# Optimization experiments

Hardware: AMD Instinct MI355X
Metric: run time of the kernel (lower is better)

## Reference

```python
import jax, jax.numpy as jnp
import numpy as np

B, T, V = 128, 128, 30000
DE, DP, PV = 300, 30, 50
H = 300
HEADS = 6
LA, LL = 5, 24
POL = 3
RED = 10
NEG = -1e9


def entmax15(x):
    # exact 1.5-entmax along last axis (sorting algorithm, Peters & Martins 2019)
    d = x.shape[-1]
    x = x / 2.0
    x = x - jnp.max(x, axis=-1, keepdims=True)
    xs = -jnp.sort(-x, axis=-1)                      # descending
    rho = jnp.arange(1, d + 1, dtype=x.dtype)
    mean = jnp.cumsum(xs, axis=-1) / rho
    meansq = jnp.cumsum(xs * xs, axis=-1) / rho
    ss = rho * (meansq - mean * mean)
    delta = (1.0 - ss) / rho
    tau = mean - jnp.sqrt(jnp.maximum(delta, 0.0))
    support = jnp.sum((tau <= xs).astype(jnp.int32), axis=-1, keepdims=True)
    tau_star = jnp.take_along_axis(tau, support - 1, axis=-1)
    return jnp.square(jnp.maximum(x - tau_star, 0.0))


def lstm_dir(x, mask, Wih, Whh, bih, bhh, reverse):
    # packed-sequence-equivalent LSTM: state frozen / output zeroed at padded steps
    b = x.shape[0]
    h0 = jnp.zeros((b, Whh.shape[1]), x.dtype)

    def step(carry, inp):
        h, c = carry
        xt, mt = inp
        g = xt @ Wih.T + h @ Whh.T + (bih + bhh)
        i, f, gg, o = jnp.split(g, 4, axis=-1)       # torch gate order i,f,g,o
        c_new = jax.nn.sigmoid(f) * c + jax.nn.sigmoid(i) * jnp.tanh(gg)
        h_new = jax.nn.sigmoid(o) * jnp.tanh(c_new)
        m = mt[:, None]
        return (jnp.where(m, h_new, h), jnp.where(m, c_new, c)), jnp.where(m, h_new, 0.0)

    _, outs = jax.lax.scan(step, (h0, h0),
                           (jnp.swapaxes(x, 0, 1), jnp.swapaxes(mask, 0, 1)),
                           reverse=reverse)
    return jnp.swapaxes(outs, 0, 1)


def se_layer(x, valid, w1, b1, w2, b2):
    # SELayer over the SEQUENCE dim (channel == max_len); x: [b,t,d], valid: [b,t]
    y = jnp.mean(x, axis=-1)                         # adaptive avg-pool over (1, d)
    y = jax.nn.relu(y @ w1.T + b1) @ w2.T + b2
    y = y + jnp.where(valid > 0, 0.0, NEG)           # mask_2
    y = jax.nn.softmax(y, axis=1)
    return x * y[..., None]


def gcn(x, A, W, b):
    # D @ A @ D @ x @ W + b with D = diag((rowsum(A)+1)^-0.5)
    dn = (jnp.sum(A, axis=2) + 1.0) ** -0.5
    An = dn[:, :, None] * A * dn[:, None, :]
    return jnp.einsum('bij,bjd->bid', An, x) @ W + b


def _forward(text_indices, aspect_indices, left_indices, pos_indices, asp_post, height,
             adj, embed_matrix, pos_emb_w, Wih_f, Whh_f, bih_f, bhh_f,
             Wih_b, Whh_b, bih_b, bhh_b, wq, bq, wk, bk,
             se_w1, se_b1, se_w2, se_b2, gc1_w, gc1_b, gc2_w, gc2_b,
             affine1, affine2, fc_w, fc_b):
    b, t = text_indices.shape
    nonpad = text_indices != 0
    valid = nonpad.astype(jnp.float32)               # mask_ squeezed -> [b,t]
    text_len = jnp.sum(nonpad, axis=-1)
    aspect_real_len = jnp.sum(aspect_indices != 0, axis=-1)
    left_len = jnp.sum(left_indices != 0, axis=-1)   # aspect_double_idx = [left_len,left_len]

    # embedding; overwrite aspect position with mean aspect embedding
    text = embed_matrix[text_indices]
    am = (aspect_indices != 0).astype(jnp.float32)[..., None]
    asp_mean = jnp.sum(embed_matrix[aspect_indices] * am, axis=1) / aspect_real_len[:, None].astype(jnp.float32)
    text = text.at[jnp.arange(b), asp_post].set(asp_mean)
    embs = jnp.concatenate([text, pos_emb_w[pos_indices]], axis=-1)

    lenmask = jnp.arange(t)[None, :] < text_len[:, None]
    text_out = jnp.concatenate([
        lstm_dir(embs, lenmask, Wih_f, Whh_f, bih_f, bhh_f, False),
        lstm_dir(embs, lenmask, Wih_b, Whh_b, bih_b, bhh_b, True)], axis=-1)  # [b,t,2H]

    # multi-head entmax attention -> semantic adjacency
    dk = (2 * H) // HEADS
    q = (text_out @ wq.T + bq).reshape(b, t, HEADS, dk).transpose(0, 2, 1, 3)
    k = (text_out @ wk.T + bk).reshape(b, t, HEADS, dk).transpose(0, 2, 1, 3)
    scores = jnp.einsum('bhqd,bhkd->bhqk', q, k) / (dk ** 0.5)
    scores = jnp.where(nonpad[:, None, None, :], scores, NEG)
    adj_sem = jnp.mean(entmax15(scores), axis=1)     # average over heads
    eye = jnp.eye(t, dtype=adj_sem.dtype)
    adj_sem = adj_sem * (1.0 - eye) + eye            # zero diagonal, add identity
    adj_sem = valid[:, :, None] * adj_sem

    se = lambda z: se_layer(z, valid, se_w1, se_b1, se_w2, se_b2)
    # (the first x = relu(gc1(..,adj)); x = relu(gc2(..,adj)) branch is dead code:
    #  x is overwritten before use, so only the x_sem path matters)
    x_sem = jax.nn.relu(gcn(se(text_out), adj_sem, gc1_w, gc1_b))
    x = jax.nn.relu(gcn(se(x_sem), adj, gc2_w, gc2_b))

    A1 = jax.nn.softmax(jnp.einsum('bid,bjd->bij', x @ affine1, x_sem), axis=-1)
    A2 = jax.nn.softmax(jnp.einsum('bid,bjd->bij', x_sem @ affine2, x), axis=-1)
    out = jnp.concatenate([jnp.einsum('bij,bjd->bid', A1, x_sem),
                           jnp.einsum('bij,bjd->bid', A2, x)], axis=-1)  # [b,t,4H]
    aspmask = (jnp.arange(t)[None, :] == left_len[:, None]).astype(jnp.float32)
    pooled = jnp.sum(out * aspmask[..., None], axis=1)  # keep aspect token only
    return pooled @ fc_w + fc_b                         # [b, POL]


def setup_inputs():
    key = jax.random.key(0)
    ks = jax.random.split(key, 36)
    f32 = jnp.float32
    pos_t = jnp.arange(T)[None, :]
    text_len = jax.random.randint(ks[0], (B,), T // 2, T + 1)
    text_indices = jax.random.randint(ks[1], (B, T), 1, V) * (pos_t < text_len[:, None])
    asp_len = jax.random.randint(ks[2], (B,), 1, LA + 1)
    aspect_indices = jax.random.randint(ks[3], (B, LA), 1, V) * (jnp.arange(LA)[None, :] < asp_len[:, None])
    left_len = jax.random.randint(ks[4], (B,), 1, LL + 1)
    left_indices = jax.random.randint(ks[5], (B, LL), 1, V) * (jnp.arange(LL)[None, :] < left_len[:, None])
    pos_indices = jax.random.randint(ks[6], (B, T), 1, PV) * (pos_t < text_len[:, None])
    vmask = (pos_t < text_len[:, None]).astype(f32)
    adj = (jax.random.uniform(ks[7], (B, T, T)) < 0.08).astype(f32)
    adj = adj * vmask[:, :, None] * vmask[:, None, :]
    asp_post = left_len                              # aspect sits right after left context
    height = jax.random.randint(ks[8], (B, T + 1), 1, 12)

    def rn(k, shape, scale=0.05):
        return jax.random.normal(k, shape, dtype=f32) * scale

    params = dict(
        embed_matrix=rn(ks[9], (V, DE), 0.5),
        pos_emb_w=rn(ks[10], (PV, DP), 0.5).at[0].set(0.0),
        Wih_f=rn(ks[11], (4 * H, DE + DP)), Whh_f=rn(ks[12], (4 * H, H)),
        bih_f=rn(ks[13], (4 * H,)), bhh_f=rn(ks[14], (4 * H,)),
        Wih_b=rn(ks[15], (4 * H, DE + DP)), Whh_b=rn(ks[16], (4 * H, H)),
        bih_b=rn(ks[17], (4 * H,)), bhh_b=rn(ks[18], (4 * H,)),
        wq=rn(ks[19], (2 * H, 2 * H)), bq=rn(ks[20], (2 * H,)),
        wk=rn(ks[21], (2 * H, 2 * H)), bk=rn(ks[22], (2 * H,)),
        se_w1=rn(ks[23], (T // RED, T)), se_b1=rn(ks[24], (T // RED,)),
        se_w2=rn(ks[25], (T, T // RED)), se_b2=rn(ks[26], (T,)),
        gc1_w=rn(ks[27], (2 * H, 2 * H)), gc1_b=rn(ks[28], (2 * H,)),
        gc2_w=rn(ks[29], (2 * H, 2 * H)), gc2_b=rn(ks[30], (2 * H,)),
        affine1=rn(ks[31], (2 * H, 2 * H)), affine2=rn(ks[32], (2 * H, 2 * H)),
        fc_w=rn(ks[33], (4 * H, POL)), fc_b=rn(ks[34], (POL,)),
    )
    return dict(text_indices=text_indices, aspect_indices=aspect_indices,
                left_indices=left_indices, pos_indices=pos_indices,
                asp_post=asp_post, height=height, adj=adj, **params)


def reference(text_indices, aspect_indices, left_indices, pos_indices, asp_post, height,
              adj, embed_matrix, pos_emb_w, Wih_f, Whh_f, bih_f, bhh_f,
              Wih_b, Whh_b, bih_b, bhh_b, wq, bq, wk, bk,
              se_w1, se_b1, se_w2, se_b2, gc1_w, gc1_b, gc2_w, gc2_b,
              affine1, affine2, fc_w, fc_b):
    return _forward(text_indices, aspect_indices, left_indices, pos_indices, asp_post, height,
                    adj, embed_matrix, pos_emb_w, Wih_f, Whh_f, bih_f, bhh_f,
                    Wih_b, Whh_b, bih_b, bhh_b, wq, bq, wk, bk,
                    se_w1, se_b1, se_w2, se_b2, gc1_w, gc1_b, gc2_w, gc2_b,
                    affine1, affine2, fc_w, fc_b)
```

## Files before the change

### kernel.cpp

```cpp
#include <hip/hip_runtime.h>

typedef unsigned short ushort_t;
typedef unsigned int   uint_t;
typedef __attribute__((ext_vector_type(8))) short short8;
typedef __attribute__((ext_vector_type(4))) float floatx4;

#define NEGV -1000000000.0f

__device__ __forceinline__ float bf2f(ushort_t h){ return __uint_as_float(((uint_t)h)<<16); }
__device__ __forceinline__ ushort_t f2bf(float f){
  uint_t u = __float_as_uint(f);
  uint_t r = u + 0x7fffu + ((u>>16)&1u);
  return (ushort_t)(r>>16);
}
__device__ __forceinline__ float wredsum(float v){ for(int o=32;o;o>>=1) v += __shfl_xor(v,o); return v; }
__device__ __forceinline__ float wredmax(float v){ for(int o=32;o;o>>=1) v = fmaxf(v,__shfl_xor(v,o)); return v; }
__device__ __forceinline__ int   wredsumi(int v){ for(int o=32;o;o>>=1) v += __shfl_xor(v,o); return v; }

__device__ __forceinline__ short8 ldg_cohr(const ushort_t* p){
  short8 r;
  asm volatile("global_load_dwordx4 %0, %1, off sc0 sc1"
               : "=&v"(r) : "v"(p) : "memory");
  return r;
}
__device__ __forceinline__ void stg_b128_cohr(ushort_t* p, short8 v){
  asm volatile("global_store_dwordx4 %0, %1, off sc0 sc1" :: "v"(p), "v"(v) : "memory");
}

__device__ __forceinline__ float fsig(float x){ return 1.f/(1.f+__expf(-x)); }
__device__ __forceinline__ float ftanh(float x){ return 1.f - 2.f/(1.f+__expf(2.f*x)); }

__global__ void k_cvt8(const void* __restrict__ src, ushort_t* __restrict__ dst,
                       long n, const ushort_t* __restrict__ probe_src){
  __shared__ int sflag;
  if (threadIdx.x < 64){
    ushort_t u = probe_src[2*threadIdx.x];
    int e = (u>>7)&0xFF;
    int c = (e>=100 && e<=140) ? 1 : 0;
    c = wredsumi(c);
    if (threadIdx.x==0) sflag = (c>32) ? 1 : 0;
  }
  __syncthreads();
  bool isbf = (sflag!=0);
  long base = (blockIdx.x*256L + threadIdx.x)*8;
  if (base>=n) return;
  if (isbf){
    if (base+8<=n) *(uint4*)(dst+base) = *(const uint4*)((const ushort_t*)src+base);
    else for (long i=base;i<n;i++) dst[i]=((const ushort_t*)src)[i];
  } else {
    const float* s = (const float*)src;
    if (base+8<=n){
      float4 v0 = *(const float4*)(s+base);
      float4 v1 = *(const float4*)(s+base+4);
      ushort_t o[8] = {f2bf(v0.x),f2bf(v0.y),f2bf(v0.z),f2bf(v0.w),
                       f2bf(v1.x),f2bf(v1.y),f2bf(v1.z),f2bf(v1.w)};
      *(uint4*)(dst+base) = *(uint4*)o;
    } else {
      for (long i=base;i<n;i++) dst[i]=f2bf(s[i]);
    }
  }
}

__device__ __forceinline__ bool probe_is_bf16(const ushort_t* probe_src){
  int c=0;
  #pragma unroll 1
  for (int i=0;i<64;i++){
    ushort_t u = probe_src[2*i];
    int e = (u>>7)&0xFF;
    c += (e>=100 && e<=140) ? 1 : 0;
  }
  return c>32;
}

__global__ void k_lens(const int* __restrict__ ti, const int* __restrict__ li,
                       int* __restrict__ nonpad, int* __restrict__ text_len,
                       int* __restrict__ left_len){
  int b = blockIdx.x, t = threadIdx.x;
  nonpad[b*128+t] = (ti[b*128+t]!=0) ? 1 : 0;
  if (t==0){
    int c=0; for (int k2=0;k2<128;k2++) c += (ti[b*128+k2]!=0);
    text_len[b]=c;
    int l=0; for (int k2=0;k2<24;k2++) l += (li[b*24+k2]!=0);
    left_len[b]=l;
  }
}

__global__ void k_aspmean(const int* __restrict__ ai, const ushort_t* __restrict__ em,
                          float* __restrict__ asp_mean){
  int b = blockIdx.x;
  int idxs[5]; int cnt=0;
  for (int a=0;a<5;a++){ int ix=ai[b*5+a]; idxs[a]=ix; cnt += (ix!=0); }
  float inv = 1.0f/(float)cnt;
  for (int d=threadIdx.x; d<300; d+=128){
    float s=0.f;
    for (int a=0;a<5;a++) if (idxs[a]) s += bf2f(em[(long)idxs[a]*300+d]);
    asp_mean[b*300+d] = s*inv;
  }
}

__global__ void k_embs(const int* __restrict__ ti, const int* __restrict__ pi,
                       const int* __restrict__ asp_post,
                       const ushort_t* __restrict__ em, const ushort_t* __restrict__ pe,
                       const float* __restrict__ asp_mean, ushort_t* __restrict__ embs){
  int blk = blockIdx.x;
  int b = blk>>7, t = blk&127;
  int ap = asp_post[b];
  int tix = ti[b*128+t];
  int pix = pi[b*128+t];
  for (int col=threadIdx.x; col<336; col+=128){
    ushort_t v;
    if (col<300) v = (t==ap) ? f2bf(asp_mean[b*300+col]) : em[(long)tix*300+col];
    else if (col<330) v = pe[pix*30 + (col-300)];
    else v = 0;
    embs[(long)(b*128+t)*336 + col] = v;
  }
}

__global__ void k_padwih2(const ushort_t* __restrict__ src, ushort_t* __restrict__ dst){
  int i = blockIdx.x*blockDim.x + threadIdx.x;
  if (i >= 1280*336) return;
  int r = i/336, k = i - r*336;
  int j = r>>2, gate = r&3;
  ushort_t v = 0;
  if (j<300 && k<330) v = src[(long)(gate*300+j)*330 + k];
  dst[i] = v;
}

__global__ void k_padwhh2(const ushort_t* __restrict__ src, ushort_t* __restrict__ dst){
  int i = blockIdx.x*blockDim.x + threadIdx.x;
  if (i >= 1280*320) return;
  int r = i/320, k = i - r*320;
  int j = r>>2, gate = r&3;
  ushort_t v = 0;
  if (j<300 && k<300) v = src[(long)(gate*300+j)*300 + k];
  dst[i] = v;
}

__global__ void k_biassum2(const ushort_t* __restrict__ a, const ushort_t* __restrict__ b,
                           float* __restrict__ dst){
  int i = blockIdx.x*blockDim.x + threadIdx.x;
  if (i>=1280) return;
  int j = i>>2, g = i&3;
  dst[i] = (j<300) ? (bf2f(a[g*300+j]) + bf2f(b[g*300+j])) : 0.f;
}

__global__ void k_biascvt(const ushort_t* __restrict__ a, float* __restrict__ dst, int n){
  int i = blockIdx.x*blockDim.x + threadIdx.x;
  if (i<n) dst[i] = bf2f(a[i]);
}

template<int TB, int MODE>
__global__ __launch_bounds__(256) void gemm_k(
    int M, int N, int K,
    const ushort_t* __restrict__ A, long lda, long sAz,
    const ushort_t* __restrict__ B, long ldb, long sBz,
    float* __restrict__ Cf, ushort_t* __restrict__ Cb, long ldc, long sCz,
    const float* __restrict__ bias, int relu,
    const float* __restrict__ rowscale,
    const int* __restrict__ nonpad)
{
  __shared__ ushort_t As[128*40];
  __shared__ ushort_t Bs[128*40];
  const int tid = threadIdx.x;
  const int m0 = blockIdx.x*128, n0 = blockIdx.y*128;
  const int z = blockIdx.z;
  const ushort_t* Ap = A + (long)z*sAz;
  const ushort_t* Bp = B + (long)z*sBz;
  floatx4 acc[4][4];
  #pragma unroll
  for (int i=0;i<4;i++)
    #pragma unroll
    for (int j=0;j<4;j++){ acc[i][j][0]=0.f; acc[i][j][1]=0.f; acc[i][j][2]=0.f; acc[i][j][3]=0.f; }
  const int w = tid>>6, wm = w&1, wn = w>>1;
  const int lane = tid&63, lr = lane&15, lq = lane>>4;

  for (int k0=0;k0<K;k0+=32){
    #pragma unroll
    for (int c2=0;c2<2;c2++){
      int ch = tid + 256*c2;
      int row = ch>>2, kc = (ch&3)*8;
      int gr = m0+row, gk = k0+kc;
      uint4 v{};
      if (gr<M && gk<K) v = *(const uint4*)(Ap + (long)gr*lda + gk);
      *(uint4*)(&As[row*40+kc]) = v;
    }
    if (TB){
      #pragma unroll
      for (int c2=0;c2<2;c2++){
        int ch = tid + 256*c2;
        int row = ch>>2, kc = (ch&3)*8;
        int gn = n0+row, gk = k0+kc;
        uint4 v{};
        if (gn<N && gk<K) v = *(const uint4*)(Bp + (long)gn*ldb + gk);
        int sw = kc ^ (((row>>3)&3)<<3);
        *(uint4*)(&Bs[row*40+sw]) = v;
      }
    } else {
      #pragma unroll
      for (int c2=0;c2<2;c2++){
        int ch = tid + 256*c2;
        int kk = ch>>4, nc = (ch&15)*8;
        int gk = k0+kk, gn = n0+nc;
        uint4 v{};
        if (gk<K && gn<N) v = *(const uint4*)(Bp + (long)gk*ldb + gn);
        uint_t wsv[4] = {v.x, v.y, v.z, v.w};
        #pragma unroll
        for (int e=0;e<8;e++){
          ushort_t hv = (e&1) ? (ushort_t)(wsv[e>>1]>>16) : (ushort_t)(wsv[e>>1]&0xffffu);
          int n = nc+e;
          int sw = kk ^ (((n>>3)&3)<<3);
          Bs[n*40+sw] = hv;
        }
      }
    }
    __syncthreads();
    short8 af[4], bfv[4];
    #pragma unroll
    for (int i=0;i<4;i++) af[i] = *(const short8*)(&As[(wm*64+i*16+lr)*40 + lq*8]);
    #pragma unroll
    for (int j=0;j<4;j++){
      int n = wn*64+j*16+lr;
      int sw = (lq*8) ^ (((n>>3)&3)<<3);
      bfv[j] = *(const short8*)(&Bs[n*40+sw]);
    }
    #pragma unroll
    for (int i=0;i<4;i++)
      #pragma unroll
      for (int j=0;j<4;j++)
        acc[i][j] = __builtin_amdgcn_mfma_f32_16x16x32_bf16(af[i], bfv[j], acc[i][j], 0,0,0);
    __syncthreads();
  }

  #pragma unroll
  for (int i=0;i<4;i++){
    #pragma unroll
    for (int j=0;j<4;j++){
      #pragma unroll
      for (int r=0;r<4;r++){
        int row = m0 + wm*64 + i*16 + lq*4 + r;
        int col = n0 + wn*64 + j*16 + lr;
        if (row<M && col<N){
          float v = acc[i][j][r];
          if (rowscale) v *= rowscale[(long)z*M + row];
          if (bias) v += bias[col];
          if (relu && v<0.f) v = 0.f;
          if (MODE==1){
            Cb[(long)z*sCz + (long)row*ldc + col] = f2bf(v);
          } else if (MODE==2){
            int b = row>>7, t = row&127;
            int h = col/100, d = col - h*100;
            Cb[ ((long)((b*6+h)*128+t))*104 + d ] = f2bf(v);
          } else if (MODE==3){
            v *= 0.1f;
            if (!nonpad[(z/6)*128 + col]) v = NEGV;
            Cf[(long)z*sCz + (long)row*ldc + col] = v;
          }
        }
      }
    }
  }
}

#define ALD 328
#define HXD 40

__global__ __launch_bounds__(512,1) void lstm2_k(
    const ushort_t* __restrict__ whh2f, const ushort_t* __restrict__ whh2b,
    const ushort_t* __restrict__ gipf, const ushort_t* __restrict__ gipb,
    ushort_t* __restrict__ hbuf,
    int* __restrict__ barr,
    ushort_t* __restrict__ text_out, const int* __restrict__ text_len)
{
  __shared__ ushort_t Alds[128*ALD];
  __shared__ ushort_t Blds[64*ALD];
  __shared__ ushort_t hx[64*HXD];

  const int bx = blockIdx.x;
  const int slice = bx % 10;
  const int grp   = bx / 10;
  const int dir = grp & 1, bh = grp >> 1;
  const ushort_t* __restrict__ whh = dir ? whh2b : whh2f;
  const ushort_t* __restrict__ gip = dir ? gipb : gipf;
  ushort_t* hb = hbuf + (long)dir * (2L*128*320);
  int* bar = barr + grp*128;

  const int tid = threadIdx.x;
  const int w = tid>>6, lane = tid&63, lr = lane&15, lq = lane>>4;
  const int wm = w&3, wn = w>>2;

  for (int i = tid; i < 128*40; i += 512){
    int row = i/40, c = (i-row*40)*8;
    uint4 v = *(const uint4*)(whh + (long)(slice*128+row)*320 + c);
    *(uint4*)(&Alds[row*ALD + c]) = v;
  }

  int jj_[2], b_[2], bl_[2], tl_[2];
  #pragma unroll
  for (int mi=0;mi<2;mi++) jj_[mi] = slice*32 + wm*8 + mi*4 + lq;
  #pragma unroll
  for (int ni=0;ni<2;ni++){
    bl_[ni] = wn*32 + ni*16 + lr;
    b_[ni]  = bh*64 + bl_[ni];
    tl_[ni] = text_len[b_[ni]];
  }

  const int aoff0 = ((wm*2+0)*16+lr)*ALD + lq*8;
  const int aoff1 = ((wm*2+1)*16+lr)*ALD + lq*8;
  const int boff0 = (wn*32+   lr)*ALD + lq*8;
  const int boff1 = (wn*32+16+lr)*ALD + lq*8;

  float    c_st[2][2];
  ushort_t h_st[2][2];
  #pragma unroll
  for (int mi=0;mi<2;mi++){ c_st[mi][0]=0.f; c_st[mi][1]=0.f; h_st[mi][0]=0; h_st[mi][1]=0; }

  __syncthreads();

  for (int s=0; s<128; s++){
    const int t = dir ? (127-s) : s;
    const ushort_t* rb = hb + (long)(s&1)*(128L*320);
    ushort_t*       wb = hb + (long)((s+1)&1)*(128L*320);

    uint2 gp[2][2];
    #pragma unroll
    for (int mi=0;mi<2;mi++)
      #pragma unroll
      for (int ni=0;ni<2;ni++)
        gp[mi][ni] = *(const uint2*)(gip + ((long)(b_[ni]*128 + t))*1280 + jj_[mi]*4);

    short8 tmp[5]; int ro_[5], ch_[5];
    #pragma unroll
    for (int k=0;k<5;k++){
      int c = tid + k*512;
      int row = c/40, ch = c - row*40;
      ro_[k]=row; ch_[k]=ch;
      tmp[k] = ldg_cohr(rb + (long)(bh*64+row)*320 + ch*8);
    }
    asm volatile("s_waitcnt vmcnt(0)" ::: "memory");
    __builtin_amdgcn_sched_barrier(0);
    #pragma unroll
    for (int k=0;k<5;k++)
      *(short8*)(&Blds[ro_[k]*ALD + ch_[k]*8]) = tmp[k];
    __syncthreads();

    floatx4 acc[2][2];
    #pragma unroll
    for (int mi=0;mi<2;mi++)
      #pragma unroll
      for (int ni=0;ni<2;ni++){ acc[mi][ni][0]=0.f; acc[mi][ni][1]=0.f; acc[mi][ni][2]=0.f; acc[mi][ni][3]=0.f; }
    #pragma unroll
    for (int kf=0;kf<10;kf++){
      short8 a0 = *(const short8*)(&Alds[aoff0 + kf*32]);
      short8 a1 = *(const short8*)(&Alds[aoff1 + kf*32]);
      short8 b0 = *(const short8*)(&Blds[boff0 + kf*32]);
      short8 b1 = *(const short8*)(&Blds[boff1 + kf*32]);
      acc[0][0] = __builtin_amdgcn_mfma_f32_16x16x32_bf16(a0, b0, acc[0][0], 0,0,0);
      acc[0][1] = __builtin_amdgcn_mfma_f32_16x16x32_bf16(a0, b1, acc[0][1], 0,0,0);
      acc[1][0] = __builtin_amdgcn_mfma_f32_16x16x32_bf16(a1, b0, acc[1][0], 0,0,0);
      acc[1][1] = __builtin_amdgcn_mfma_f32_16x16x32_bf16(a1, b1, acc[1][1], 0,0,0);
    }

    #pragma unroll
    for (int mi=0;mi<2;mi++){
      #pragma unroll
      for (int ni=0;ni<2;ni++){
        float g_i = acc[mi][ni][0] + bf2f((ushort_t)(gp[mi][ni].x & 0xffffu));
        float g_f = acc[mi][ni][1] + bf2f((ushort_t)(gp[mi][ni].x >> 16));
        float g_g = acc[mi][ni][2] + bf2f((ushort_t)(gp[mi][ni].y & 0xffffu));
        float g_o = acc[mi][ni][3] + bf2f((ushort_t)(gp[mi][ni].y >> 16));
        float ig = fsig(g_i);
        float fg = fsig(g_f);
        float gg = ftanh(g_g);
        float og = fsig(g_o);
        float cn = fg*c_st[mi][ni] + ig*gg;
        float hn = og*ftanh(cn);
        bool m = (t < tl_[ni]);
        if (m) c_st[mi][ni] = cn;
        ushort_t hv = m ? f2bf(hn) : h_st[mi][ni];
        h_st[mi][ni] = hv;
        hx[bl_[ni]*HXD + wm*8 + mi*4 + lq] = hv;
        if (jj_[mi] < 300)
          text_out[((long)(b_[ni]*128 + t))*600 + dir*300 + jj_[mi]] = m ? f2bf(hn) : (ushort_t)0;
      }
    }
    __syncthreads();

    if (tid < 256){
      int row = tid>>2, jj8 = (tid&3)*8;
      short8 hvv = *(const short8*)(&hx[row*HXD + jj8]);
      stg_b128_cohr(wb + (long)(bh*64+row)*320 + slice*32 + jj8, hvv);
    }
    asm volatile("s_waitcnt vmcnt(0)" ::: "memory");
    __syncthreads();
    if (tid==0){
      __hip_atomic_fetch_add(&bar[s], 1, __ATOMIC_RELAXED, __HIP_MEMORY_SCOPE_AGENT);
      while (__hip_atomic_load(&bar[s], __ATOMIC_RELAXED, __HIP_MEMORY_SCOPE_AGENT) < 10)
        __builtin_amdgcn_s_sleep(1);
    }
    __syncthreads();
  }
}

__global__ __launch_bounds__(64) void k_entmax(float* __restrict__ p){
  long row = blockIdx.x;
  float* base = p + row*128;
  __shared__ float xo[128], xs[128], c1[128], c2[128];
  int t = threadIdx.x;
  float a = base[t]*0.5f, b = base[t+64]*0.5f;
  float m = wredmax(fmaxf(a,b));
  a -= m; b -= m;
  xo[t]=a; xo[t+64]=b; xs[t]=a; xs[t+64]=b;
  __syncthreads();
  for (int k2=2;k2<=128;k2<<=1){
    for (int j=k2>>1;j>0;j>>=1){
      int i = ((t & ~(j-1))<<1) | (t & (j-1));
      int ixj = i | j;
      float vi = xs[i], vj = xs[ixj];
      bool blk = (i & k2)==0;
      bool sw = blk ? (vi < vj) : (vi > vj);
      __syncthreads();
      if (sw){ xs[i]=vj; xs[ixj]=vi; }
      __syncthreads();
    }
  }
  c1[t]=xs[t];       c2[t]=xs[t]*xs[t];
  c1[t+64]=xs[t+64]; c2[t+64]=xs[t+64]*xs[t+64];
  __syncthreads();
  for (int d=1; d<128; d<<=1){
    float a1 = (t>=d)     ? c1[t-d]    : 0.f;
    float a2 = (t>=d)     ? c2[t-d]    : 0.f;
    float b1 = (t+64>=d)  ? c1[t+64-d] : 0.f;
    float b2 = (t+64>=d)  ? c2[t+64-d] : 0.f;
    float x1=c1[t], y1=c2[t], x2=c1[t+64], y2=c2[t+64];
    __syncthreads();
    c1[t]=x1+a1; c2[t]=y1+a2; c1[t+64]=x2+b1; c2[t+64]=y2+b2;
    __syncthreads();
  }
  float tau_a, tau_b; int cnt=0;
  {
    float rho = (float)(t+1);
    float mean = c1[t]/rho, msq = c2[t]/rho;
    float ss = rho*(msq-mean*mean);
    float delta = (1.f-ss)/rho;
    tau_a = mean - sqrtf(fmaxf(delta,0.f));
    cnt += (tau_a <= xs[t]) ? 1 : 0;
  }
  {
    float rho = (float)(t+65);
    float mean = c1[t+64]/rho, msq = c2[t+64]/rho;
    float ss = rho*(msq-mean*mean);
    float delta = (1.f-ss)/rho;
    tau_b = mean - sqrtf(fmaxf(delta,0.f));
    cnt += (tau_b <= xs[t+64]) ? 1 : 0;
  }
  __syncthreads();
  c1[t]=tau_a; c1[t+64]=tau_b;
  __syncthreads();
  int support = wredsumi(cnt);
  support = (support<1) ? 1 : ((support>128) ? 128 : support);
  float tau_star = c1[support-1];
  float oa = fmaxf(xo[t]-tau_star, 0.f);
  float ob = fmaxf(xo[t+64]-tau_star, 0.f);
  base[t] = oa*oa; base[t+64] = ob*ob;
}

__global__ void k_adjsem(const float* __restrict__ p, const int* __restrict__ nonpad,
                         ushort_t* __restrict__ adj_sem){
  int idx = blockIdx.x*blockDim.x + threadIdx.x;
  if (idx >= 128*128*128) return;
  int b = idx>>14, rem = idx&16383, i = rem>>7, j = rem&127;
  float s = 0.f;
  for (int h=0;h<6;h++) s += p[(long)b*98304 + h*16384 + i*128 + j];
  float v = s/6.0f;
  if (i==j) v = 1.0f;
  if (!nonpad[b*128+i]) v = 0.f;
  adj_sem[idx] = f2bf(v);
}

__global__ __launch_bounds__(64) void k_dn(const ushort_t* __restrict__ src, float* __restrict__ dnv){
  long row = blockIdx.x;
  int l = threadIdx.x;
  float s = bf2f(src[row*128+l]) + bf2f(src[row*128+l+64]);
  s = wredsum(s);
  if (l==0) dnv[row] = 1.0f/sqrtf(s+1.0f);
}

__global__ __launch_bounds__(64) void k_mean(const ushort_t* __restrict__ X, float* __restrict__ ymean){
  long row = blockIdx.x;
  float s=0.f;
  for (int d=threadIdx.x; d<600; d+=64) s += bf2f(X[row*600+d]);
  s = wredsum(s);
  if (threadIdx.x==0) ymean[row] = s/600.0f;
}

__global__ void k_senet(const float* __restrict__ ymean,
                        const ushort_t* __restrict__ w1, const ushort_t* __restrict__ b1,
                        const ushort_t* __restrict__ w2, const ushort_t* __restrict__ b2,
                        const int* __restrict__ nonpad, float* __restrict__ ysoft){
  int b = blockIdx.x, t = threadIdx.x;
  __shared__ float yv[128], z1[12], red[128];
  yv[t] = ymean[b*128+t];
  __syncthreads();
  if (t<12){
    float s = bf2f(b1[t]);
    for (int k2=0;k2<128;k2++) s += yv[k2]*bf2f(w1[t*128+k2]);
    z1[t] = fmaxf(s,0.f);
  }
  __syncthreads();
  float v = bf2f(b2[t]);
  for (int r=0;r<12;r++) v += z1[r]*bf2f(w2[t*12+r]);
  if (!nonpad[b*128+t]) v += NEGV;
  red[t]=v; __syncthreads();
  for (int s2=64;s2>0;s2>>=1){ if (t<s2) red[t]=fmaxf(red[t],red[t+s2]); __syncthreads(); }
  float mx = red[0]; __syncthreads();
  float e = expf(v-mx);
  red[t]=e; __syncthreads();
  for (int s2=64;s2>0;s2>>=1){ if (t<s2) red[t]+=red[t+s2]; __syncthreads(); }
  float sm = red[0];
  ysoft[b*128+t] = e/sm;
}

__global__ void k_scale2(const ushort_t* __restrict__ X, const float* __restrict__ ysoft,
                         const float* __restrict__ dnv, ushort_t* __restrict__ out){
  int i = blockIdx.x*blockDim.x + threadIdx.x;
  if (i >= 128*128*600) return;
  int row = i/600;
  out[i] = f2bf(bf2f(X[i])*ysoft[row]*dnv[row]);
}

__global__ void k_gather(const ushort_t* __restrict__ X, const int* __restrict__ left_len,
                         ushort_t* __restrict__ dst){
  int b = blockIdx.x;
  int lb = left_len[b];
  for (int d=threadIdx.x; d<600; d+=128)
    dst[b*600+d] = X[(long)(b*128+lb)*600+d];
}

__global__ __launch_bounds__(256) void k_pool(const ushort_t* __restrict__ g,
                                              const ushort_t* __restrict__ X,
                                              float* __restrict__ pooled, int poff){
  int b = blockIdx.x, tid = threadIdx.x;
  __shared__ float gs[600], sbuf[128], red[256];
  for (int d=tid; d<600; d+=256) gs[d] = bf2f(g[b*600+d]);
  __syncthreads();
  int wv = tid>>6, lane = tid&63;
  for (int jj=wv; jj<128; jj+=4){
    float s=0.f;
    for (int d=lane; d<600; d+=64) s += gs[d]*bf2f(X[(long)(b*128+jj)*600+d]);
    s = wredsum(s);
    if (lane==0) sbuf[jj]=s;
  }
  __syncthreads();
  float v = (tid<128) ? sbuf[tid] : -3.4e38f;
  red[tid]=v; __syncthreads();
  for (int s2=128;s2>0;s2>>=1){ if (tid<s2) red[tid]=fmaxf(red[tid],red[tid+s2]); __syncthreads(); }
  float mx = red[0]; __syncthreads();
  float e = (tid<128) ? expf(v-mx) : 0.f;
  red[tid]=e; __syncthreads();
  for (int s2=128;s2>0;s2>>=1){ if (tid<s2) red[tid]+=red[tid+s2]; __syncthreads(); }
  float sm = red[0]; __syncthreads();
  if (tid<128) sbuf[tid] = e/sm;
  __syncthreads();
  for (int d=tid; d<600; d+=256){
    float acc=0.f;
    for (int j=0;j<128;j++) acc += sbuf[j]*bf2f(X[(long)(b*128+j)*600+d]);
    pooled[(long)b*1200 + poff + d] = acc;
  }
}

__global__ __launch_bounds__(64) void k_final(const float* __restrict__ pooled,
                                              const ushort_t* __restrict__ fcw,
                                              const ushort_t* __restrict__ fcb,
                                              void* __restrict__ out,
                                              const ushort_t* __restrict__ probe_src){
  bool isbf = probe_is_bf16(probe_src);
  int b = blockIdx.x, lane = threadIdx.x;
  for (int p=0;p<3;p++){
    float s=0.f;
    for (int d=lane; d<1200; d+=64) s += pooled[(long)b*1200+d]*bf2f(fcw[d*3+p]);
    s = wredsum(s);
    if (lane==0){
      float r = s + bf2f(fcb[p]);
      if (isbf) ((ushort_t*)out)[b*3+p] = f2bf(r);
      else      ((float*)out)[b*3+p] = r;
    }
  }
}

extern "C" void kernel_launch(void* const* d_in, const int* in_sizes, int n_in,
                              void* d_out, int out_size, void* d_ws, size_t ws_size,
                              hipStream_t stream) {
  const int*      ti   = (const int*)d_in[0];
  const int*      ai   = (const int*)d_in[1];
  const int*      li   = (const int*)d_in[2];
  const int*      pi   = (const int*)d_in[3];
  const int*      aps  = (const int*)d_in[4];
  const ushort_t* probe = (const ushort_t*)d_in[7];

  char* w = (char*)d_ws; size_t off = 0;
  auto alloc = [&](size_t bytes)->char*{ char* p = w+off; off = (off+bytes+255)&~(size_t)255; return p; };

  int*   text_len = (int*)alloc(512);
  int*   left_len = (int*)alloc(512);
  int*   nonpad   = (int*)alloc(65536);
  float* asp_mean = (float*)alloc(153600);
  float* dn1      = (float*)alloc(65536);
  float* dn2      = (float*)alloc(65536);
  float* ymean    = (float*)alloc(65536);
  float* ysoft    = (float*)alloc(65536);
  ushort_t* wihpf = (ushort_t*)alloc(860160);
  ushort_t* wihpb = (ushort_t*)alloc(860160);
  ushort_t* whh2f = (ushort_t*)alloc(819200);
  ushort_t* whh2b = (ushort_t*)alloc(819200);
  ushort_t* hbuf  = (ushort_t*)alloc(327680);
  int*      barr  = (int*)alloc(2048);
  float* biasgf   = (float*)alloc(5120);
  float* biasgb   = (float*)alloc(5120);
  float* bqf      = (float*)alloc(2400);
  float* bkf      = (float*)alloc(2400);
  float* gc1bf    = (float*)alloc(2400);
  float* gc2bf    = (float*)alloc(2400);
  ushort_t* g1    = (ushort_t*)alloc(153600);
  ushort_t* g2    = (ushort_t*)alloc(153600);
  ushort_t* xr    = (ushort_t*)alloc(153600);
  ushort_t* xsr   = (ushort_t*)alloc(153600);
  float* pooled   = (float*)alloc(614400);
  ushort_t* adj_c  = (ushort_t*)alloc(4194304);
  ushort_t* pe_c   = (ushort_t*)alloc(2048);
  ushort_t* wihf_c = (ushort_t*)alloc(792000);
  ushort_t* wihb_c = (ushort_t*)alloc(792000);
  ushort_t* whhf_c = (ushort_t*)alloc(720000);
  ushort_t* whhb_c = (ushort_t*)alloc(720000);
  ushort_t* bihf_c = (ushort_t*)alloc(2400);
  ushort_t* bhhf_c = (ushort_t*)alloc(2400);
  ushort_t* bihb_c = (ushort_t*)alloc(2400);
  ushort_t* bhhb_c = (ushort_t*)alloc(2400);
  ushort_t* wq_c   = (ushort_t*)alloc(720000);
  ushort_t* bq_c   = (ushort_t*)alloc(1200);
  ushort_t* wk_c   = (ushort_t*)alloc(720000);
  ushort_t* bk_c   = (ushort_t*)alloc(1200);
  ushort_t* sw1_c  = (ushort_t*)alloc(3072);
  ushort_t* sb1_c  = (ushort_t*)alloc(256);
  ushort_t* sw2_c  = (ushort_t*)alloc(3072);
  ushort_t* sb2_c  = (ushort_t*)alloc(256);
  ushort_t* g1w_c  = (ushort_t*)alloc(720000);
  ushort_t* g1b_c  = (ushort_t*)alloc(1200);
  ushort_t* g2w_c  = (ushort_t*)alloc(720000);
  ushort_t* g2b_c  = (ushort_t*)alloc(1200);
  ushort_t* af1_c  = (ushort_t*)alloc(720000);
  ushort_t* af2_c  = (ushort_t*)alloc(720000);
  ushort_t* fcw_c  = (ushort_t*)alloc(7200);
  ushort_t* fcb_c  = (ushort_t*)alloc(256);
  ushort_t* embs  = (ushort_t*)alloc(11010048);
  ushort_t* textout = (ushort_t*)alloc(19660800);
  char* R = alloc(95420416);
  ushort_t* em_c    = (ushort_t*)(R);
  ushort_t* gip_f   = (ushort_t*)(R);
  ushort_t* gip_b   = (ushort_t*)(R+41943040);
  ushort_t* qh      = (ushort_t*)(R);
  ushort_t* kh      = (ushort_t*)(R+20447232);
  float*    scores  = (float*)(R+40894464);
  ushort_t* adj_sem = (ushort_t*)(R+91226112);
  ushort_t* se_x    = (ushort_t*)(R+40894464);
  ushort_t* Zb      = (ushort_t*)(R+60555264);
  ushort_t* x_sem   = (ushort_t*)(R);
  ushort_t* xb      = (ushort_t*)(R+20447232);
  (void)ws_size; (void)n_in; (void)in_sizes; (void)out_size;

  {
    const int idx[27] = {7,6, 8,9,13,10,14,11,12,15,16,17,18,19,20,21,22,23,24,25,26,27,28,29,30,31,32};
    ushort_t* dl[27] = {em_c,adj_c, pe_c,wihf_c,wihb_c,whhf_c,whhb_c,bihf_c,bhhf_c,bihb_c,bhhb_c,
                        wq_c,bq_c,wk_c,bk_c,sw1_c,sb1_c,sw2_c,sb2_c,
                        g1w_c,g1b_c,g2w_c,g2b_c,af1_c,af2_c,fcw_c,fcb_c};
    const long nl[27] = {9000000L,2097152L, 900,396000,396000,360000,360000,1200,1200,1200,1200,
                         360000,600,360000,600,1536,12,1536,128,
                         360000,600,360000,600,360000,360000,3600,3};
    for (int i=0;i<27;i++){
      long nb = ((nl[i]+7)/8 + 255)/256;
      k_cvt8<<<(int)nb,256,0,stream>>>(d_in[idx[i]], dl[i], nl[i], probe);
    }
  }

  k_lens<<<128,128,0,stream>>>(ti, li, nonpad, text_len, left_len);
  k_aspmean<<<128,128,0,stream>>>(ai, em_c, asp_mean);
  k_embs<<<16384,128,0,stream>>>(ti, pi, aps, em_c, pe_c, asp_mean, embs);
  k_padwih2<<<(1280*336+255)/256,256,0,stream>>>(wihf_c, wihpf);
  k_padwih2<<<(1280*336+255)/256,256,0,stream>>>(wihb_c, wihpb);
  k_padwhh2<<<(1280*320+255)/256,256,0,stream>>>(whhf_c, whh2f);
  k_padwhh2<<<(1280*320+255)/256,256,0,stream>>>(whhb_c, whh2b);
  k_biassum2<<<(1280+255)/256,256,0,stream>>>(bihf_c, bhhf_c, biasgf);
  k_biassum2<<<(1280+255)/256,256,0,stream>>>(bihb_c, bhhb_c, biasgb);
  k_biascvt<<<3,256,0,stream>>>(bq_c, bqf, 600);
  k_biascvt<<<3,256,0,stream>>>(bk_c, bkf, 600);
  k_biascvt<<<3,256,0,stream>>>(g1b_c, gc1bf, 600);
  k_biascvt<<<3,256,0,stream>>>(g2b_c, gc2bf, 600);

  gemm_k<1,1><<<dim3(128,10,1),256,0,stream>>>(16384,1280,336, embs,336,0, wihpf,336,0,
        nullptr, gip_f,1280,0, biasgf,0,nullptr,nullptr);
  gemm_k<1,1><<<dim3(128,10,1),256,0,stream>>>(16384,1280,336, embs,336,0, wihpb,336,0,
        nullptr, gip_b,1280,0, biasgb,0,nullptr,nullptr);

  hipMemsetAsync(hbuf, 0, 327680, stream);
  hipMemsetAsync(barr, 0, 2048, stream);
  lstm2_k<<<40,512,0,stream>>>(whh2f, whh2b, gip_f, gip_b, hbuf, barr, textout, text_len);

  hipMemsetAsync(qh, 0, 20447232, stream);
  hipMemsetAsync(kh, 0, 20447232, stream);
  gemm_k<1,2><<<dim3(128,5,1),256,0,stream>>>(16384,600,600, textout,600,0, wq_c,600,0,
        nullptr, qh,0,0, bqf,0,nullptr,nullptr);
  gemm_k<1,2><<<dim3(128,5,1),256,0,stream>>>(16384,600,600, textout,600,0, wk_c,600,0,
        nullptr, kh,0,0, bkf,0,nullptr,nullptr);

  gemm_k<1,3><<<dim3(1,1,768),256,0,stream>>>(128,128,104, qh,104,13312, kh,104,13312,
        scores, nullptr, 128, 16384, nullptr,0,nullptr, nonpad);

  k_entmax<<<98304,64,0,stream>>>(scores);

  k_adjsem<<<(2097152+255)/256,256,0,stream>>>(scores, nonpad, adj_sem);
  k_dn<<<16384,64,0,stream>>>(adj_sem, dn1);
  k_dn<<<16384,64,0,stream>>>(adj_c, dn2);

  k_mean<<<16384,64,0,stream>>>(textout, ymean);
  k_senet<<<128,128,0,stream>>>(ymean, sw1_c,sb1_c,sw2_c,sb2_c, nonpad, ysoft);
  k_scale2<<<(9830400+255)/256,256,0,stream>>>(textout, ysoft, dn1, se_x);
  gemm_k<0,1><<<dim3(1,5,128),256,0,stream>>>(128,600,128, adj_sem,128,16384, se_x,600,76800,
        nullptr, Zb,600,76800, nullptr,0, dn1, nullptr);
  gemm_k<0,1><<<dim3(128,5,1),256,0,stream>>>(16384,600,600, Zb,600,0, g1w_c,600,0,
        nullptr, x_sem,600,0, gc1bf,1,nullptr,nullptr);

  k_mean<<<16384,64,0,stream>>>(x_sem, ymean);
  k_senet<<<128,128,0,stream>>>(ymean, sw1_c,sb1_c,sw2_c,sb2_c, nonpad, ysoft);
  k_scale2<<<(9830400+255)/256,256,0,stream>>>(x_sem, ysoft, dn2, se_x);
  gemm_k<0,1><<<dim3(1,5,128),256,0,stream>>>(128,600,128, adj_c,128,16384, se_x,600,76800,
        nullptr, Zb,600,76800, nullptr,0, dn2, nullptr);
  gemm_k<0,1><<<dim3(128,5,1),256,0,stream>>>(16384,600,600, Zb,600,0, g2w_c,600,0,
        nullptr, xb,600,0, gc2bf,1,nullptr,nullptr);

  k_gather<<<128,128,0,stream>>>(xb, left_len, xr);
  k_gather<<<128,128,0,stream>>>(x_sem, left_len, xsr);
  gemm_k<0,1><<<dim3(1,5,1),256,0,stream>>>(128,600,600, xr,600,0, af1_c,600,0,
        nullptr, g1,600,0, nullptr,0,nullptr,nullptr);
  gemm_k<0,1><<<dim3(1,5,1),256,0,stream>>>(128,600,600, xsr,600,0, af2_c,600,0,
        nullptr, g2,600,0, nullptr,0,nullptr,nullptr);
  k_pool<<<128,256,0,stream>>>(g1, x_sem, pooled, 0);
  k_pool<<<128,256,0,stream>>>(g2, xb, pooled, 600);

  k_final<<<128,64,0,stream>>>(pooled, fcw_c, fcb_c, d_out, probe);
}
```

Measured before the change: 1.867 ms.

## Keep LSTM recurrent weights in registers and prefetch next-step gate inputs

The persistent LSTM kernel now loads each wave's slice of the recurrent weight matrix into registers once, instead of staging it in LDS and reading it back every step. The per-step precomputed gate inputs for the next timestep are prefetched at the end of the current step, so that load overlaps the barrier wait. The text_out stores are made unconditional through a dummy buffer, so the s_waitcnt can use a fixed count, vmcnt(8), and no longer drains them. The goal is to shorten the serial per-step critical path, at the cost of higher register pressure and reliance on an exact in-flight memory operation count.

```diff
diff --git a/kernel.cpp b/kernel.cpp
--- a/kernel.cpp
+++ b/kernel.cpp
@@ -261,7 +261,7 @@
   }
 }
 
-#define ALD 328
+#define BLD 328
 #define HXD 40
 
 __global__ __launch_bounds__(512,1) void lstm2_k(
@@ -269,10 +269,10 @@
     const ushort_t* __restrict__ gipf, const ushort_t* __restrict__ gipb,
     ushort_t* __restrict__ hbuf,
     int* __restrict__ barr,
-    ushort_t* __restrict__ text_out, const int* __restrict__ text_len)
+    ushort_t* __restrict__ text_out, const int* __restrict__ text_len,
+    ushort_t* __restrict__ dumpb)
 {
-  __shared__ ushort_t Alds[128*ALD];
-  __shared__ ushort_t Blds[64*ALD];
+  __shared__ ushort_t Blds[64*BLD];
   __shared__ ushort_t hx[64*HXD];
 
   const int bx = blockIdx.x;
@@ -288,11 +288,18 @@
   const int w = tid>>6, lane = tid&63, lr = lane&15, lq = lane>>4;
   const int wm = w&3, wn = w>>2;
 
-  for (int i = tid; i < 128*40; i += 512){
-    int row = i/40, c = (i-row*40)*8;
-    uint4 v = *(const uint4*)(whh + (long)(slice*128+row)*320 + c);
-    *(uint4*)(&Alds[row*ALD + c]) = v;
-  }
+  short8 a[2][10];
+  #pragma unroll
+  for (int mi=0;mi<2;mi++){
+    const ushort_t* ar = whh + (long)(slice*128 + (wm*2+mi)*16 + lr)*320 + lq*8;
+    #pragma unroll
+    for (int kf=0;kf<10;kf++) a[mi][kf] = *(const short8*)(ar + kf*32);
+  }
+  #pragma unroll
+  for (int mi=0;mi<2;mi++)
+    #pragma unroll
+    for (int kf=0;kf<10;kf++)
+      asm volatile("" : "+v"(a[mi][kf]));
 
   int jj_[2], b_[2], bl_[2], tl_[2];
   #pragma unroll
@@ -304,29 +311,28 @@
     tl_[ni] = text_len[b_[ni]];
   }
 
-  const int aoff0 = ((wm*2+0)*16+lr)*ALD + lq*8;
-  const int aoff1 = ((wm*2+1)*16+lr)*ALD + lq*8;
-  const int boff0 = (wn*32+   lr)*ALD + lq*8;
-  const int boff1 = (wn*32+16+lr)*ALD + lq*8;
+  const int boff0 = (wn*32+   lr)*BLD + lq*8;
+  const int boff1 = (wn*32+16+lr)*BLD + lq*8;
 
   float    c_st[2][2];
   ushort_t h_st[2][2];
   #pragma unroll
   for (int mi=0;mi<2;mi++){ c_st[mi][0]=0.f; c_st[mi][1]=0.f; h_st[mi][0]=0; h_st[mi][1]=0; }
 
-  __syncthreads();
+  uint2 gp[2][2];
+  {
+    int t0 = dir ? 127 : 0;
+    #pragma unroll
+    for (int mi=0;mi<2;mi++)
+      #pragma unroll
+      for (int ni=0;ni<2;ni++)
+        gp[mi][ni] = *(const uint2*)(gip + ((long)(b_[ni]*128 + t0))*1280 + jj_[mi]*4);
+  }
 
   for (int s=0; s<128; s++){
     const int t = dir ? (127-s) : s;
     const ushort_t* rb = hb + (long)(s&1)*(128L*320);
     ushort_t*       wb = hb + (long)((s+1)&1)*(128L*320);
-
-    uint2 gp[2][2];
-    #pragma unroll
-    for (int mi=0;mi<2;mi++)
-      #pragma unroll
-      for (int ni=0;ni<2;ni++)
-        gp[mi][ni] = *(const uint2*)(gip + ((long)(b_[ni]*128 + t))*1280 + jj_[mi]*4);
 
     short8 tmp[5]; int ro_[5], ch_[5];
     #pragma unroll
@@ -340,7 +346,7 @@
     __builtin_amdgcn_sched_barrier(0);
     #pragma unroll
     for (int k=0;k<5;k++)
-      *(short8*)(&Blds[ro_[k]*ALD + ch_[k]*8]) = tmp[k];
+      *(short8*)(&Blds[ro_[k]*BLD + ch_[k]*8]) = tmp[k];
     __syncthreads();
 
     floatx4 acc[2][2];
@@ -350,16 +356,15 @@
       for (int ni=0;ni<2;ni++){ acc[mi][ni][0]=0.f; acc[mi][ni][1]=0.f; acc[mi][ni][2]=0.f; acc[mi][ni][3]=0.f; }
     #pragma unroll
     for (int kf=0;kf<10;kf++){
-      short8 a0 = *(const short8*)(&Alds[aoff0 + kf*32]);
-      short8 a1 = *(const short8*)(&Alds[aoff1 + kf*32]);
       short8 b0 = *(const short8*)(&Blds[boff0 + kf*32]);
       short8 b1 = *(const short8*)(&Blds[boff1 + kf*32]);
-      acc[0][0] = __builtin_amdgcn_mfma_f32_16x16x32_bf16(a0, b0, acc[0][0], 0,0,0);
-      acc[0][1] = __builtin_amdgcn_mfma_f32_16x16x32_bf16(a0, b1, acc[0][1], 0,0,0);
-      acc[1][0] = __builtin_amdgcn_mfma_f32_16x16x32_bf16(a1, b0, acc[1][0], 0,0,0);
-      acc[1][1] = __builtin_amdgcn_mfma_f32_16x16x32_bf16(a1, b1, acc[1][1], 0,0,0);
-    }
-
+      acc[0][0] = __builtin_amdgcn_mfma_f32_16x16x32_bf16(a[0][kf], b0, acc[0][0], 0,0,0);
+      acc[0][1] = __builtin_amdgcn_mfma_f32_16x16x32_bf16(a[0][kf], b1, acc[0][1], 0,0,0);
+      acc[1][0] = __builtin_amdgcn_mfma_f32_16x16x32_bf16(a[1][kf], b0, acc[1][0], 0,0,0);
+      acc[1][1] = __builtin_amdgcn_mfma_f32_16x16x32_bf16(a[1][kf], b1, acc[1][1], 0,0,0);
+    }
+
+    ushort_t tov[2][2];
     #pragma unroll
     for (int mi=0;mi<2;mi++){
       #pragma unroll
@@ -379,8 +384,7 @@
         ushort_t hv = m ? f2bf(hn) : h_st[mi][ni];
         h_st[mi][ni] = hv;
         hx[bl_[ni]*HXD + wm*8 + mi*4 + lq] = hv;
-        if (jj_[mi] < 300)
-          text_out[((long)(b_[ni]*128 + t))*600 + dir*300 + jj_[mi]] = m ? f2bf(hn) : (ushort_t)0;
+        tov[mi][ni] = m ? f2bf(hn) : (ushort_t)0;
       }
     }
     __syncthreads();
@@ -390,7 +394,24 @@
       short8 hvv = *(const short8*)(&hx[row*HXD + jj8]);
       stg_b128_cohr(wb + (long)(bh*64+row)*320 + slice*32 + jj8, hvv);
     }
-    asm volatile("s_waitcnt vmcnt(0)" ::: "memory");
+    #pragma unroll
+    for (int mi=0;mi<2;mi++)
+      #pragma unroll
+      for (int ni=0;ni<2;ni++){
+        ushort_t* toa = (jj_[mi] < 300)
+          ? &text_out[((long)(b_[ni]*128 + t))*600 + dir*300 + jj_[mi]]
+          : &dumpb[tid*4 + mi*2 + ni];
+        *toa = tov[mi][ni];
+      }
+    {
+      int tn = dir ? ((s<127) ? (126-s) : 127) : ((s<127) ? (s+1) : 0);
+      #pragma unroll
+      for (int mi=0;mi<2;mi++)
+        #pragma unroll
+        for (int ni=0;ni<2;ni++)
+          gp[mi][ni] = *(const uint2*)(gip + ((long)(b_[ni]*128 + tn))*1280 + jj_[mi]*4);
+    }
+    asm volatile("s_waitcnt vmcnt(8)" ::: "memory");
     __syncthreads();
     if (tid==0){
       __hip_atomic_fetch_add(&bar[s], 1, __ATOMIC_RELAXED, __HIP_MEMORY_SCOPE_AGENT);
@@ -614,6 +635,7 @@
   ushort_t* whh2b = (ushort_t*)alloc(819200);
   ushort_t* hbuf  = (ushort_t*)alloc(327680);
   int*      barr  = (int*)alloc(2048);
+  ushort_t* dumpb = (ushort_t*)alloc(4096);
   float* biasgf   = (float*)alloc(5120);
   float* biasgb   = (float*)alloc(5120);
   float* bqf      = (float*)alloc(2400);
@@ -702,7 +724,7 @@
 
   hipMemsetAsync(hbuf, 0, 327680, stream);
   hipMemsetAsync(barr, 0, 2048, stream);
-  lstm2_k<<<40,512,0,stream>>>(whh2f, whh2b, gip_f, gip_b, hbuf, barr, textout, text_len);
+  lstm2_k<<<40,512,0,stream>>>(whh2f, whh2b, gip_f, gip_b, hbuf, barr, textout, text_len, dumpb);
 
   hipMemsetAsync(qh, 0, 20447232, stream);
   hipMemsetAsync(kh, 0, 20447232, stream);
```

Result: no change. 1.865 ms (-0.1%).
